# Optimization experiments

Measured on AMD Instinct MI355X. Metric: run time of the kernel, lower is better.

The kernel has to match this reference:

```python
import jax, jax.numpy as jnp
import numpy as np

D_MODEL = 256; N_LAYERS = 4; INPUT_LEN = 15
D_INNER = 512; D_STATE = 16; D_CONV = 4; DT_RANK = 16
BATCH = 4; SEQ = 2048; EPS = 1e-5

def _ln(x, w, b):
    m = jnp.mean(x, -1, keepdims=True)
    v = jnp.var(x, -1, keepdims=True)
    return (x - m) * jax.lax.rsqrt(v + EPS) * w + b

def _silu(x):
    return x * jax.nn.sigmoid(x)

def _mixer(h, inW, cw, cb, xpW, dtW, dtb, A_log, Dp, opW):
    # h: [B,L,d_model]
    xz = h @ inW.T                      # [B,L,2*D_INNER]
    xh, z = jnp.split(xz, 2, axis=-1)
    # causal depthwise conv1d
    xc = jnp.transpose(xh, (0, 2, 1))   # [B,D,L]
    xc = jax.lax.conv_general_dilated(xc, cw, (1,), [(D_CONV - 1, 0)],
                                      feature_group_count=D_INNER,
                                      dimension_numbers=('NCH', 'OIH', 'NCH'))
    xc = xc + cb[None, :, None]
    xh = _silu(jnp.transpose(xc, (0, 2, 1)))  # [B,L,D]
    dbl = xh @ xpW.T                    # [B,L,DT_RANK+2N]
    dt = dbl[..., :DT_RANK]
    Bm = dbl[..., DT_RANK:DT_RANK + D_STATE]
    C = dbl[..., DT_RANK + D_STATE:]
    dt = jax.nn.softplus(dt @ dtW.T + dtb)    # [B,L,D]
    A = -jnp.exp(A_log)                       # [D,N]
    dA = jnp.exp(dt[..., None] * A)           # [B,L,D,N]
    dBu = dt[..., None] * Bm[:, :, None, :] * xh[..., None]  # [B,L,D,N]
    def step(hst, inp):
        dA_t, dBu_t, C_t = inp
        hst = dA_t * hst + dBu_t
        y = jnp.einsum('bdn,bn->bd', hst, C_t)
        return hst, y
    h0 = jnp.zeros((xh.shape[0], D_INNER, D_STATE), xh.dtype)
    _, ys = jax.lax.scan(step, h0, (jnp.transpose(dA, (1, 0, 2, 3)),
                                    jnp.transpose(dBu, (1, 0, 2, 3)),
                                    jnp.transpose(C, (1, 0, 2))))
    y = jnp.transpose(ys, (1, 0, 2)) + Dp * xh
    y = y * _silu(z)
    return y @ opW.T

def setup_inputs():
    key = jax.random.key(0)
    ks = jax.random.split(key, 8)
    s = 0.02
    return {
        'x_src': jax.random.normal(ks[0], (BATCH, SEQ, INPUT_LEN), jnp.float32),
        'single_eval_pos': 1024,
        'in_W': jax.random.normal(ks[1], (D_MODEL, INPUT_LEN)) * s,
        'norm_w': jnp.ones((N_LAYERS, D_MODEL)),
        'norm_b': jnp.zeros((N_LAYERS, D_MODEL)),
        'inproj_W': jax.random.normal(ks[2], (N_LAYERS, 2 * D_INNER, D_MODEL)) * s,
        'conv_w': jax.random.normal(ks[3], (N_LAYERS, D_INNER, 1, D_CONV)) * 0.2,
        'conv_b': jnp.zeros((N_LAYERS, D_INNER)),
        'xproj_W': jax.random.normal(ks[4], (N_LAYERS, DT_RANK + 2 * D_STATE, D_INNER)) * s,
        'dtproj_W': jax.random.normal(ks[5], (N_LAYERS, D_INNER, DT_RANK)) * 0.1,
        'dtproj_b': jnp.log(jnp.expm1(jnp.full((N_LAYERS, D_INNER), 0.01))),
        'A_log': jnp.log(jnp.broadcast_to(jnp.arange(1, D_STATE + 1, dtype=jnp.float32), (N_LAYERS, D_INNER, D_STATE)) + 0.0),
        'D_param': jnp.ones((N_LAYERS, D_INNER)),
        'outproj_W': jax.random.normal(ks[6], (N_LAYERS, D_MODEL, D_INNER)) * s,
        'out_W': jax.random.normal(ks[7], (1, D_MODEL)) * s,
    }

def reference(x_src, single_eval_pos, in_W, norm_w, norm_b, inproj_W, conv_w, conv_b, xproj_W, dtproj_W, dtproj_b, A_log, D_param, outproj_W, out_W):
    h = x_src @ in_W.T                  # [B,L,d_model]
    res = None
    for i in range(N_LAYERS):
        res = h if res is None else h + res
        hn = _ln(res, norm_w[i], norm_b[i])
        h = _mixer(hn, inproj_W[i], conv_w[i], conv_b[i], xproj_W[i],
                   dtproj_W[i], dtproj_b[i], A_log[i], D_param[i], outproj_W[i])
    # backbone returns hidden_states directly (norm_f defined but not applied)
    return h @ out_W.T                  # [B,L,1]
```

## Files before the change

kernel.cpp:

```cpp
#include <hip/hip_runtime.h>

#define B_   4
#define T_   2048
#define BT_  8192
#define INL  15
#define DM   256
#define DI   512
#define DX   1024
#define DS_  16
#define DR_  16
#define NO_  48
#define NL   4
#define NC_  128
#define LCH  16

typedef short bf16x8 __attribute__((ext_vector_type(8)));
typedef float f32x4  __attribute__((ext_vector_type(4)));

__device__ __forceinline__ float sigmoidf_(float x){
    return __builtin_amdgcn_rcpf(1.f + __expf(-x));
}
__device__ __forceinline__ float softplusf_(float x){
    return fmaxf(x, 0.f) + __logf(1.f + __expf(-fabsf(x)));
}

__device__ __forceinline__ unsigned short f2bf(float x){
    union { float f; unsigned u; } v; v.f = x;
    unsigned r = (v.u + 0x7FFFu + ((v.u >> 16) & 1u)) >> 16;
    return (unsigned short)r;
}
__device__ __forceinline__ float bf2f(unsigned short h){
    union { unsigned u; float f; } v; v.u = ((unsigned)h) << 16;
    return v.f;
}

__device__ __forceinline__ void ld16(const float* __restrict__ p, float* v){
    const float4* q = (const float4*)p;
    float4 x0=q[0],x1=q[1],x2=q[2],x3=q[3];
    v[0]=x0.x; v[1]=x0.y; v[2]=x0.z; v[3]=x0.w;
    v[4]=x1.x; v[5]=x1.y; v[6]=x1.z; v[7]=x1.w;
    v[8]=x2.x; v[9]=x2.y; v[10]=x2.z; v[11]=x2.w;
    v[12]=x3.x; v[13]=x3.y; v[14]=x3.z; v[15]=x3.w;
}
__device__ __forceinline__ void st16(float* __restrict__ p, const float* v){
    float4* q = (float4*)p;
    q[0] = make_float4(v[0],v[1],v[2],v[3]);
    q[1] = make_float4(v[4],v[5],v[6],v[7]);
    q[2] = make_float4(v[8],v[9],v[10],v[11]);
    q[3] = make_float4(v[12],v[13],v[14],v[15]);
}

__global__ void k_cvtW3(const float* __restrict__ W0, unsigned short* __restrict__ h0,
                        unsigned short* __restrict__ l0, int n0,
                        const float* __restrict__ W1, unsigned short* __restrict__ h1,
                        unsigned short* __restrict__ l1, int n1,
                        const float* __restrict__ W2, unsigned short* __restrict__ h2,
                        unsigned short* __restrict__ l2, int n2){
    int g = blockIdx.x*256 + threadIdx.x;
    const float* W; unsigned short *hi, *lo; int idx;
    if(g < n0){ W = W0; hi = h0; lo = l0; idx = g; }
    else if(g < n0+n1){ W = W1; hi = h1; lo = l1; idx = g - n0; }
    else if(g < n0+n1+n2){ W = W2; hi = h2; lo = l2; idx = g - n0 - n1; }
    else return;
    float4 v = ((const float4*)W)[idx];
    ushort4 h, l;
    h.x = f2bf(v.x); l.x = f2bf(v.x - bf2f(h.x));
    h.y = f2bf(v.y); l.y = f2bf(v.y - bf2f(h.y));
    h.z = f2bf(v.z); l.z = f2bf(v.z - bf2f(h.z));
    h.w = f2bf(v.w); l.w = f2bf(v.w - bf2f(h.w));
    ((ushort4*)hi)[idx] = h;
    ((ushort4*)lo)[idx] = l;
}

__global__ void k_wcomb(const float* __restrict__ opW, const float* __restrict__ outW,
                        float* __restrict__ cw){
    int k = blockIdx.x*256 + threadIdx.x;
    float s = 0.f;
#pragma unroll 8
    for(int m=0;m<DM;m++) s += outW[m]*opW[(size_t)m*DI + k];
    cw[k] = s;
}

__global__ void k_inln(const float* __restrict__ x, const float* __restrict__ W,
                       float* __restrict__ res,
                       unsigned short* __restrict__ hnhi, unsigned short* __restrict__ hnlo,
                       const float* __restrict__ w, const float* __restrict__ b){
    int wv = threadIdx.x >> 6, lane = threadIdx.x & 63;
    int bt = blockIdx.x*4 + wv;
    const float* xr = x + bt*INL;
    float xl[INL];
#pragma unroll
    for(int k=0;k<INL;k++) xl[k] = xr[k];
    float4 v;
    float* vv = (float*)&v;
#pragma unroll
    for(int j=0;j<4;j++){
        int m = lane*4 + j;
        const float* wr = W + m*INL;
        float acc = 0.f;
#pragma unroll
        for(int k=0;k<INL;k++) acc += xl[k]*wr[k];
        vv[j] = acc;
    }
    ((float4*)(res + (size_t)bt*DM))[lane] = v;
    float s  = v.x+v.y+v.z+v.w;
    float ss = v.x*v.x+v.y*v.y+v.z*v.z+v.w*v.w;
#pragma unroll
    for(int m=1;m<64;m<<=1){ s += __shfl_xor(s,m); ss += __shfl_xor(ss,m); }
    float mean = s*(1.f/DM);
    float var  = ss*(1.f/DM) - mean*mean;
    float inv  = rsqrtf(var + 1e-5f);
    float4 wt = ((const float4*)w)[lane];
    float4 bs = ((const float4*)b)[lane];
    float4 o;
    o.x = (v.x-mean)*inv*wt.x + bs.x;
    o.y = (v.y-mean)*inv*wt.y + bs.y;
    o.z = (v.z-mean)*inv*wt.z + bs.z;
    o.w = (v.w-mean)*inv*wt.w + bs.w;
    ushort4 hh, ll;
    hh.x = f2bf(o.x); ll.x = f2bf(o.x - bf2f(hh.x));
    hh.y = f2bf(o.y); ll.y = f2bf(o.y - bf2f(hh.y));
    hh.z = f2bf(o.z); ll.z = f2bf(o.z - bf2f(hh.z));
    hh.w = f2bf(o.w); ll.w = f2bf(o.w - bf2f(hh.w));
    ((ushort4*)(hnhi + (size_t)bt*DM))[lane] = hh;
    ((ushort4*)(hnlo + (size_t)bt*DM))[lane] = ll;
}

__global__ void k_resln(const float* __restrict__ h, float* __restrict__ res,
                        unsigned short* __restrict__ hnhi, unsigned short* __restrict__ hnlo,
                        const float* __restrict__ w, const float* __restrict__ b, int storeRes){
    int wv = threadIdx.x >> 6, lane = threadIdx.x & 63;
    int bt = blockIdx.x*4 + wv;
    float4 v = ((const float4*)(h + (size_t)bt*DM))[lane];
    {
        float4 r = ((const float4*)(res + (size_t)bt*DM))[lane];
        v.x+=r.x; v.y+=r.y; v.z+=r.z; v.w+=r.w;
    }
    if(storeRes)
        ((float4*)(res + (size_t)bt*DM))[lane] = v;
    float s  = v.x+v.y+v.z+v.w;
    float ss = v.x*v.x+v.y*v.y+v.z*v.z+v.w*v.w;
#pragma unroll
    for(int m=1;m<64;m<<=1){ s += __shfl_xor(s,m); ss += __shfl_xor(ss,m); }
    float mean = s*(1.f/DM);
    float var  = ss*(1.f/DM) - mean*mean;
    float inv  = rsqrtf(var + 1e-5f);
    float4 wt = ((const float4*)w)[lane];
    float4 bs = ((const float4*)b)[lane];
    float4 o;
    o.x = (v.x-mean)*inv*wt.x + bs.x;
    o.y = (v.y-mean)*inv*wt.y + bs.y;
    o.z = (v.z-mean)*inv*wt.z + bs.z;
    o.w = (v.w-mean)*inv*wt.w + bs.w;
    ushort4 hh, ll;
    hh.x = f2bf(o.x); ll.x = f2bf(o.x - bf2f(hh.x));
    hh.y = f2bf(o.y); ll.y = f2bf(o.y - bf2f(hh.y));
    hh.z = f2bf(o.z); ll.z = f2bf(o.z - bf2f(hh.z));
    hh.w = f2bf(o.w); ll.w = f2bf(o.w - bf2f(hh.w));
    ((ushort4*)(hnhi + (size_t)bt*DM))[lane] = hh;
    ((ushort4*)(hnlo + (size_t)bt*DM))[lane] = ll;
}

template<int BM,int BN>
__global__ void __launch_bounds__(256) k_gemm_bf3(
    const unsigned short* __restrict__ Ahi, const unsigned short* __restrict__ Alo,
    const unsigned short* __restrict__ Bhi, const unsigned short* __restrict__ Blo,
    float* __restrict__ C, int M, int N, int K)
{
    constexpr int LDP = 40;
    constexpr int WM = BM/2, WN = BN/2;
    constexpr int MI_ = WM/16, NI_ = WN/16;
    __shared__ unsigned short sAh[BM*LDP], sAl[BM*LDP], sBh[BN*LDP], sBl[BN*LDP];
    int tid  = threadIdx.x;
    int wave = tid >> 6, lane = tid & 63;
    int wm0  = (wave >> 1) * WM, wn0 = (wave & 1) * WN;
    int m0   = blockIdx.y * BM, n0 = blockIdx.x * BN;
    int lr   = lane & 15;
    int kq   = (lane >> 4) * 8;
    int quad4 = (lane >> 4) * 4;

    f32x4 acc[MI_][NI_];
#pragma unroll
    for(int i=0;i<MI_;i++)
#pragma unroll
        for(int j=0;j<NI_;j++) acc[i][j] = (f32x4){0.f,0.f,0.f,0.f};

    for(int k0=0;k0<K;k0+=32){
#pragma unroll
        for(int i=tid;i<BM*4;i+=256){
            int r = i>>2, cg = (i&3)*8;
            size_t go = (size_t)(m0+r)*K + k0 + cg;
            *(float4*)(&sAh[r*LDP + cg]) = *(const float4*)(Ahi + go);
            *(float4*)(&sAl[r*LDP + cg]) = *(const float4*)(Alo + go);
        }
#pragma unroll
        for(int i=tid;i<BN*4;i+=256){
            int r = i>>2, cg = (i&3)*8;
            size_t go = (size_t)(n0+r)*K + k0 + cg;
            *(float4*)(&sBh[r*LDP + cg]) = *(const float4*)(Bhi + go);
            *(float4*)(&sBl[r*LDP + cg]) = *(const float4*)(Blo + go);
        }
        __syncthreads();
        bf16x8 ah[MI_], al[MI_], bh[NI_], bl[NI_];
#pragma unroll
        for(int mi=0;mi<MI_;mi++){
            int ro = (wm0 + mi*16 + lr)*LDP + kq;
            ah[mi] = *(const bf16x8*)(&sAh[ro]);
            al[mi] = *(const bf16x8*)(&sAl[ro]);
        }
#pragma unroll
        for(int ni=0;ni<NI_;ni++){
            int ro = (wn0 + ni*16 + lr)*LDP + kq;
            bh[ni] = *(const bf16x8*)(&sBh[ro]);
            bl[ni] = *(const bf16x8*)(&sBl[ro]);
        }
#pragma unroll
        for(int mi=0;mi<MI_;mi++)
#pragma unroll
            for(int ni=0;ni<NI_;ni++){
                acc[mi][ni] = __builtin_amdgcn_mfma_f32_16x16x32_bf16(ah[mi], bh[ni], acc[mi][ni], 0,0,0);
                acc[mi][ni] = __builtin_amdgcn_mfma_f32_16x16x32_bf16(ah[mi], bl[ni], acc[mi][ni], 0,0,0);
                acc[mi][ni] = __builtin_amdgcn_mfma_f32_16x16x32_bf16(al[mi], bh[ni], acc[mi][ni], 0,0,0);
            }
        __syncthreads();
    }
#pragma unroll
    for(int mi=0;mi<MI_;mi++)
#pragma unroll
        for(int ni=0;ni<NI_;ni++){
            int col = n0 + wn0 + ni*16 + lr;
#pragma unroll
            for(int r=0;r<4;r++){
                int row = m0 + wm0 + mi*16 + quad4 + r;
                C[(size_t)row*N + col] = acc[mi][ni][r];
            }
        }
}

template<int BM,int BN>
__global__ void __launch_bounds__(256) k_gemm_pk(
    const unsigned* __restrict__ Apk,
    const unsigned short* __restrict__ Bhi, const unsigned short* __restrict__ Blo,
    float* __restrict__ C, int M, int N, int K)
{
    constexpr int LDP = 40;
    constexpr int WM = BM/2, WN = BN/2;
    constexpr int MI_ = WM/16, NI_ = WN/16;
    __shared__ unsigned short sAh[BM*LDP], sAl[BM*LDP], sBh[BN*LDP], sBl[BN*LDP];
    int tid  = threadIdx.x;
    int wave = tid >> 6, lane = tid & 63;
    int wm0  = (wave >> 1) * WM, wn0 = (wave & 1) * WN;
    int m0   = blockIdx.y * BM, n0 = blockIdx.x * BN;
    int lr   = lane & 15;
    int kq   = (lane >> 4) * 8;
    int quad4 = (lane >> 4) * 4;

    f32x4 acc[MI_][NI_];
#pragma unroll
    for(int i=0;i<MI_;i++)
#pragma unroll
        for(int j=0;j<NI_;j++) acc[i][j] = (f32x4){0.f,0.f,0.f,0.f};

    for(int k0=0;k0<K;k0+=32){
#pragma unroll
        for(int i=tid;i<BM*2;i+=256){
            int r = i>>1, hf = (i&1)*16;
            const uint4* yp = (const uint4*)(Apk + (size_t)(m0+r)*K + k0 + hf);
#pragma unroll
            for(int q=0;q<4;q++){
                uint4 p = yp[q];
                ushort4 H, L;
                H.x=(unsigned short)p.x;  L.x=(unsigned short)(p.x>>16);
                H.y=(unsigned short)p.y;  L.y=(unsigned short)(p.y>>16);
                H.z=(unsigned short)p.z;  L.z=(unsigned short)(p.z>>16);
                H.w=(unsigned short)p.w;  L.w=(unsigned short)(p.w>>16);
                *(ushort4*)(&sAh[r*LDP + hf + q*4]) = H;
                *(ushort4*)(&sAl[r*LDP + hf + q*4]) = L;
            }
        }
#pragma unroll
        for(int i=tid;i<BN*4;i+=256){
            int r = i>>2, cg = (i&3)*8;
            size_t go = (size_t)(n0+r)*K + k0 + cg;
            *(float4*)(&sBh[r*LDP + cg]) = *(const float4*)(Bhi + go);
            *(float4*)(&sBl[r*LDP + cg]) = *(const float4*)(Blo + go);
        }
        __syncthreads();
        bf16x8 ah[MI_], al[MI_], bh[NI_], bl[NI_];
#pragma unroll
        for(int mi=0;mi<MI_;mi++){
            int ro = (wm0 + mi*16 + lr)*LDP + kq;
            ah[mi] = *(const bf16x8*)(&sAh[ro]);
            al[mi] = *(const bf16x8*)(&sAl[ro]);
        }
#pragma unroll
        for(int ni=0;ni<NI_;ni++){
            int ro = (wn0 + ni*16 + lr)*LDP + kq;
            bh[ni] = *(const bf16x8*)(&sBh[ro]);
            bl[ni] = *(const bf16x8*)(&sBl[ro]);
        }
#pragma unroll
        for(int mi=0;mi<MI_;mi++)
#pragma unroll
            for(int ni=0;ni<NI_;ni++){
                acc[mi][ni] = __builtin_amdgcn_mfma_f32_16x16x32_bf16(ah[mi], bh[ni], acc[mi][ni], 0,0,0);
                acc[mi][ni] = __builtin_amdgcn_mfma_f32_16x16x32_bf16(ah[mi], bl[ni], acc[mi][ni], 0,0,0);
                acc[mi][ni] = __builtin_amdgcn_mfma_f32_16x16x32_bf16(al[mi], bh[ni], acc[mi][ni], 0,0,0);
            }
        __syncthreads();
    }
#pragma unroll
    for(int mi=0;mi<MI_;mi++)
#pragma unroll
        for(int ni=0;ni<NI_;ni++){
            int col = n0 + wn0 + ni*16 + lr;
#pragma unroll
            for(int r=0;r<4;r++){
                int row = m0 + wm0 + mi*16 + quad4 + r;
                C[(size_t)row*N + col] = acc[mi][ni][r];
            }
        }
}

__global__ void __launch_bounds__(512) k_convxp2(
    const float* __restrict__ xz, const float* __restrict__ cw, const float* __restrict__ cb,
    const unsigned short* __restrict__ Bhi, const unsigned short* __restrict__ Blo,
    const float* __restrict__ dtW, const float* __restrict__ dtbias,
    const float* __restrict__ A_log,
    float* __restrict__ dbl,
    float* __restrict__ S, float* __restrict__ sdt)
{
    __shared__ unsigned short sAh[16*520], sAl[16*520];
    __shared__ float sP[6][16][20];
    __shared__ float sD[16*52];

    int tid = threadIdx.x;
    int wave = tid >> 6, lane = tid & 63;
    int lr = lane & 15, kq = (lane>>4)*8, quad4 = (lane>>4)*4;
    int m0 = blockIdx.x * LCH;
    int d  = tid;
    int nt = wave >> 1, kh = wave & 1;

    float xv[19];
    {
        int rbase = m0 - 3;
        bool mask0 = ((m0 & (T_-1)) == 0);
#pragma unroll
        for(int j=0;j<19;j++)
            xv[j] = (mask0 && j<3) ? 0.f : xz[(size_t)(rbase+j)*DX + d];
    }
    float a_[16]; ld16(A_log + (size_t)d*16, a_);
    float wr_[16]; ld16(dtW + (size_t)d*16, wr_);
    float bsv = dtbias[d];
    float4 w4 = *(const float4*)(cw + d*4);
    float bias = cb[d];
    float vh[16];
#pragma unroll
    for(int t=0;t<16;t++){
        float a = bias + w4.x*xv[t] + w4.y*xv[t+1] + w4.z*xv[t+2] + w4.w*xv[t+3];
        float v = a * sigmoidf_(a);
        vh[t] = v;
        unsigned short hh = f2bf(v);
        sAh[t*520 + d] = hh;
        sAl[t*520 + d] = f2bf(v - bf2f(hh));
    }
    __syncthreads();

    if(wave < 6){
        const unsigned short* bhp = Bhi + (size_t)(nt*16 + lr)*DI + kh*256 + kq;
        const unsigned short* blp = Blo + (size_t)(nt*16 + lr)*DI + kh*256 + kq;
        f32x4 acc = {0.f,0.f,0.f,0.f};
#pragma unroll 4
        for(int ks=0;ks<8;ks++){
            int ao = lr*520 + kh*256 + ks*32 + kq;
            bf16x8 ah = *(const bf16x8*)(&sAh[ao]);
            bf16x8 al = *(const bf16x8*)(&sAl[ao]);
            bf16x8 bh = *(const bf16x8*)(bhp + ks*32);
            bf16x8 bl = *(const bf16x8*)(blp + ks*32);
            acc = __builtin_amdgcn_mfma_f32_16x16x32_bf16(ah, bh, acc, 0,0,0);
            acc = __builtin_amdgcn_mfma_f32_16x16x32_bf16(ah, bl, acc, 0,0,0);
            acc = __builtin_amdgcn_mfma_f32_16x16x32_bf16(al, bh, acc, 0,0,0);
        }
#pragma unroll
        for(int r=0;r<4;r++) sP[wave][quad4+r][lr] = acc[r];
    }
    __syncthreads();

    for(int i=tid;i<768;i+=512){
        int t = i/48, n = i - t*48;
        int nt2 = n >> 4, nn = n & 15;
        float v = sP[nt2*2][t][nn] + sP[nt2*2+1][t][nn];
        dbl[(size_t)(m0+t)*48 + n] = v;
        sD[t*52 + n] = v;
    }
    __syncthreads();

#pragma unroll
    for(int n=0;n<16;n++) a_[n] = -__expf(a_[n]);
    int b = m0 >> 11;
    int c = (m0 & (T_-1)) >> 4;
    float st_[16];
#pragma unroll
    for(int n=0;n<16;n++) st_[n] = 0.f;
    float sd = 0.f;
#pragma unroll 4
    for(int t=0;t<16;t++){
        float dl[16]; ld16(&sD[t*52], dl);
        float bv[16]; ld16(&sD[t*52 + 16], bv);
        float pre = bsv;
#pragma unroll
        for(int r=0;r<16;r++) pre += dl[r]*wr_[r];
        float dtv = softplusf_(pre);
        float dx = dtv*vh[t];
        sd += dtv;
#pragma unroll
        for(int n=0;n<16;n++) st_[n] = __expf(dtv*a_[n])*st_[n] + dx*bv[n];
    }
    st16(S + (((size_t)b*NC_ + c)*DI + d)*16, st_);
    sdt[((size_t)b*NC_ + c)*DI + d] = sd;
}

__global__ void k_scan2(const float* __restrict__ S, const float* __restrict__ sdt,
                        const float* __restrict__ A_log, float* __restrict__ Hinit){
    int g = blockIdx.x*256 + threadIdx.x;
    int b = g >> 13;
    int dn = g & 8191;
    int d = dn >> 4;
    float a = -__expf(A_log[dn]);
    float H = 0.f;
    for(int c0=0;c0<NC_;c0+=8){
        float sv[8], gv[8];
#pragma unroll
        for(int j=0;j<8;j++){
            sv[j] = S[((size_t)(b*NC_ + c0 + j))*8192 + dn];
            gv[j] = sdt[(size_t)(b*NC_ + c0 + j)*DI + d];
        }
#pragma unroll
        for(int j=0;j<8;j++){
            size_t o = ((size_t)(b*NC_ + c0 + j))*8192 + dn;
            Hinit[o] = H;
            H = __expf(gv[j]*a)*H + sv[j];
        }
    }
}

__global__ void __launch_bounds__(256) k_scan3(
    const float* __restrict__ dbl, const float* __restrict__ xz,
    const float* __restrict__ cvw, const float* __restrict__ cvb,
    const float* __restrict__ A_log, const float* __restrict__ Dpar,
    const float* __restrict__ dtW, const float* __restrict__ dtbias,
    const float* __restrict__ Hinit, unsigned* __restrict__ Y)
{
    __shared__ float sbc[16*52];
    int tid = threadIdx.x;
    int c = blockIdx.y, b = blockIdx.z;
    int m0 = b*T_ + c*LCH;
    if(tid < 192){
        int t = tid/12, s = tid - t*12;
        *(float4*)(&sbc[t*52 + s*4]) = *(const float4*)(dbl + (size_t)(m0+t)*48 + s*4);
    }
    __syncthreads();
    int d = blockIdx.x*256 + tid;
    float xv[19];
    {
        int rbase = m0 - 3;
        bool mask0 = (c == 0);
#pragma unroll
        for(int j=0;j<19;j++)
            xv[j] = (mask0 && j<3) ? 0.f : xz[(size_t)(rbase+j)*DX + d];
    }
    float zvp[16];
#pragma unroll
    for(int t=0;t<16;t++) zvp[t] = xz[(size_t)(m0+t)*DX + DI + d];
    float4 w4 = *(const float4*)(cvw + d*4);
    float bias = cvb[d];
    float xhp[16];
#pragma unroll
    for(int t=0;t<16;t++){
        float a = bias + w4.x*xv[t] + w4.y*xv[t+1] + w4.z*xv[t+2] + w4.w*xv[t+3];
        xhp[t] = a * sigmoidf_(a);
    }
    float a_[16]; ld16(A_log + (size_t)d*16, a_);
#pragma unroll
    for(int n=0;n<16;n++) a_[n] = -__expf(a_[n]);
    float wr_[16]; ld16(dtW + (size_t)d*16, wr_);
    float bsv = dtbias[d];
    float st_[16]; ld16(Hinit + (((size_t)b*NC_ + c)*DI + d)*16, st_);
    float Dp = Dpar[d];
#pragma unroll 2
    for(int t=0;t<LCH;t++){
        int bt = m0 + t;
        float dl[16]; ld16(&sbc[t*52], dl);
        float bv[16]; ld16(&sbc[t*52 + 16], bv);
        float cv[16]; ld16(&sbc[t*52 + 32], cv);
        float pre = bsv;
#pragma unroll
        for(int r=0;r<16;r++) pre += dl[r]*wr_[r];
        float dtv = softplusf_(pre);
        float xhv = xhp[t];
        float dx = dtv*xhv;
        float y = 0.f;
#pragma unroll
        for(int n=0;n<16;n++){
            st_[n] = __expf(dtv*a_[n])*st_[n] + dx*bv[n];
            y += st_[n]*cv[n];
        }
        float zv = zvp[t];
        y += Dp*xhv;
        y = y * zv * sigmoidf_(zv);
        unsigned short hh = f2bf(y);
        unsigned short ll = f2bf(y - bf2f(hh));
        Y[(size_t)bt*DI + d] = (unsigned)hh | ((unsigned)ll << 16);
    }
}

__global__ void __launch_bounds__(512) k_scan3o(
    const float* __restrict__ dbl, const float* __restrict__ xz,
    const float* __restrict__ cvw, const float* __restrict__ cvb,
    const float* __restrict__ A_log, const float* __restrict__ Dpar,
    const float* __restrict__ dtW, const float* __restrict__ dtbias,
    const float* __restrict__ Hinit, const float* __restrict__ cwc,
    float* __restrict__ out)
{
    __shared__ float sbc[16*52];
    __shared__ float sW[8][16];
    int tid = threadIdx.x;
    int c = blockIdx.x, b = blockIdx.y;
    int m0 = b*T_ + c*LCH;
    if(tid < 192){
        int t = tid/12, s = tid - t*12;
        *(float4*)(&sbc[t*52 + s*4]) = *(const float4*)(dbl + (size_t)(m0+t)*48 + s*4);
    }
    __syncthreads();
    int d = tid;
    int wave = tid >> 6, lane = tid & 63;
    float xv[19];
    {
        int rbase = m0 - 3;
        bool mask0 = (c == 0);
#pragma unroll
        for(int j=0;j<19;j++)
            xv[j] = (mask0 && j<3) ? 0.f : xz[(size_t)(rbase+j)*DX + d];
    }
    float zvp[16];
#pragma unroll
    for(int t=0;t<16;t++) zvp[t] = xz[(size_t)(m0+t)*DX + DI + d];
    float4 w4 = *(const float4*)(cvw + d*4);
    float bias = cvb[d];
    float xhp[16];
#pragma unroll
    for(int t=0;t<16;t++){
        float a = bias + w4.x*xv[t] + w4.y*xv[t+1] + w4.z*xv[t+2] + w4.w*xv[t+3];
        xhp[t] = a * sigmoidf_(a);
    }
    float a_[16]; ld16(A_log + (size_t)d*16, a_);
#pragma unroll
    for(int n=0;n<16;n++) a_[n] = -__expf(a_[n]);
    float wr_[16]; ld16(dtW + (size_t)d*16, wr_);
    float bsv = dtbias[d];
    float st_[16]; ld16(Hinit + (((size_t)b*NC_ + c)*DI + d)*16, st_);
    float Dp = Dpar[d];
    float cwv = cwc[d];
#pragma unroll 2
    for(int t=0;t<LCH;t++){
        float dl[16]; ld16(&sbc[t*52], dl);
        float bv[16]; ld16(&sbc[t*52 + 16], bv);
        float cv[16]; ld16(&sbc[t*52 + 32], cv);
        float pre = bsv;
#pragma unroll
        for(int r=0;r<16;r++) pre += dl[r]*wr_[r];
        float dtv = softplusf_(pre);
        float xhv = xhp[t];
        float dx = dtv*xhv;
        float y = 0.f;
#pragma unroll
        for(int n=0;n<16;n++){
            st_[n] = __expf(dtv*a_[n])*st_[n] + dx*bv[n];
            y += st_[n]*cv[n];
        }
        float zv = zvp[t];
        y += Dp*xhv;
        y = y * zv * sigmoidf_(zv);
        float s = y * cwv;
#pragma unroll
        for(int m=1;m<64;m<<=1) s += __shfl_xor(s,m);
        if(lane==0) sW[wave][t] = s;
    }
    __syncthreads();
    if(tid < 16){
        float s = 0.f;
#pragma unroll
        for(int w=0;w<8;w++) s += sW[w][tid];
        out[m0 + tid] = s;
    }
}

extern "C" void kernel_launch(void* const* d_in, const int* in_sizes, int n_in,
                              void* d_out, int out_size, void* d_ws, size_t ws_size,
                              hipStream_t stream){
    const float* x_src    = (const float*)d_in[0];
    const float* in_W     = (const float*)d_in[2];
    const float* norm_w   = (const float*)d_in[3];
    const float* norm_b   = (const float*)d_in[4];
    const float* inproj_W = (const float*)d_in[5];
    const float* conv_w   = (const float*)d_in[6];
    const float* conv_b   = (const float*)d_in[7];
    const float* xproj_W  = (const float*)d_in[8];
    const float* dtproj_W = (const float*)d_in[9];
    const float* dtproj_b = (const float*)d_in[10];
    const float* A_log    = (const float*)d_in[11];
    const float* D_param  = (const float*)d_in[12];
    const float* outproj_W= (const float*)d_in[13];
    const float* out_W    = (const float*)d_in[14];

    float* ws  = (float*)d_ws;
    float* h    = ws;
    float* res  = h    + (size_t)BT_*DM;
    float* xz   = res  + (size_t)BT_*DM;
    float* dbl  = xz   + (size_t)BT_*DX;
    float* sdtb = dbl  + (size_t)BT_*48;
    float* Sbuf = sdtb + (size_t)B_*NC_*DI;
    float* Hbuf = Sbuf + (size_t)B_*NC_*DI*DS_;
    unsigned short* us = (unsigned short*)(Hbuf + (size_t)B_*NC_*DI*DS_);
    unsigned short* WhiIn  = us;
    unsigned short* WloIn  = WhiIn  + (size_t)NL*DX*DM;
    unsigned short* WhiOut = WloIn  + (size_t)NL*DX*DM;
    unsigned short* WloOut = WhiOut + (size_t)NL*DM*DI;
    unsigned short* WhiXp  = WloOut + (size_t)NL*DM*DI;
    unsigned short* WloXp  = WhiXp  + (size_t)NL*NO_*DI;
    unsigned short* hnhi   = WloXp  + (size_t)NL*NO_*DI;
    unsigned short* hnlo   = hnhi   + (size_t)BT_*DM;
    unsigned*       ybuf   = (unsigned*)(hnlo + (size_t)BT_*DM);
    float*          cwb    = (float*)(ybuf + (size_t)BT_*DI);

    int n0 = NL*DX*DM/4, n1 = NL*DM*DI/4, n2 = NL*NO_*DI/4;
    k_cvtW3<<<(n0+n1+n2 + 255)/256, 256, 0, stream>>>(
        inproj_W,  WhiIn,  WloIn,  n0,
        outproj_W, WhiOut, WloOut, n1,
        xproj_W,   WhiXp,  WloXp,  n2);
    k_wcomb<<<2, 256, 0, stream>>>(outproj_W + (size_t)3*DM*DI, out_W, cwb);
    k_inln<<<BT_/4, 256, 0, stream>>>(x_src, in_W, res, hnhi, hnlo, norm_w, norm_b);
    for(int i=0;i<NL;i++){
        if(i > 0)
            k_resln<<<BT_/4, 256, 0, stream>>>(h, res, hnhi, hnlo,
                norm_w + i*DM, norm_b + i*DM, (i < NL-1) ? 1 : 0);
        k_gemm_bf3<128,128><<<dim3(DX/128, BT_/128), 256, 0, stream>>>(
            hnhi, hnlo, WhiIn + (size_t)i*DX*DM, WloIn + (size_t)i*DX*DM, xz, BT_, DX, DM);
        k_convxp2<<<BT_/LCH, 512, 0, stream>>>(xz, conv_w + i*DI*4, conv_b + i*DI,
            WhiXp + (size_t)i*NO_*DI, WloXp + (size_t)i*NO_*DI,
            dtproj_W + (size_t)i*DI*DR_, dtproj_b + i*DI,
            A_log + (size_t)i*DI*DS_, dbl, Sbuf, sdtb);
        k_scan2<<<B_*DI*DS_/256, 256, 0, stream>>>(Sbuf, sdtb, A_log + (size_t)i*DI*DS_, Hbuf);
        if(i < NL-1){
            k_scan3<<<dim3(2, NC_, B_), 256, 0, stream>>>(dbl, xz,
                conv_w + i*DI*4, conv_b + i*DI,
                A_log + (size_t)i*DI*DS_, D_param + i*DI,
                dtproj_W + (size_t)i*DI*DR_, dtproj_b + i*DI, Hbuf, ybuf);
            k_gemm_pk<128,64><<<dim3(DM/64, BT_/128), 256, 0, stream>>>(
                ybuf, WhiOut + (size_t)i*DM*DI, WloOut + (size_t)i*DM*DI, h, BT_, DM, DI);
        } else {
            k_scan3o<<<dim3(NC_, B_), 512, 0, stream>>>(dbl, xz,
                conv_w + i*DI*4, conv_b + i*DI,
                A_log + (size_t)i*DI*DS_, D_param + i*DI,
                dtproj_W + (size_t)i*DI*DR_, dtproj_b + i*DI, Hbuf, cwb,
                (float*)d_out);
        }
    }
}
```

Baseline: 553.6 us.

## Fuse out-projection GEMM with residual add and LayerNorm; merge weight-combine into convert kernel

The out-projection GEMM now computes full 256-wide rows per block (32 rows by 256 columns), stages the results in XOR-swizzled shared memory, and applies the residual add plus the next layer's LayerNorm in its epilogue, writing the bf16 hi/lo split directly. This removes the separate k_resln launch and the round trip of the h buffer through global memory each layer. The small k_wcomb kernel is folded into the tail blocks of the weight-conversion kernel to save a launch. The trade-off is a narrower M tile, so every block reloads the full 256x512 B matrix, and a grid of 256 blocks may underfill the GPU.

```diff
diff --git a/kernel.cpp b/kernel.cpp
--- a/kernel.cpp
+++ b/kernel.cpp
@@ -55,13 +55,24 @@
                         const float* __restrict__ W1, unsigned short* __restrict__ h1,
                         unsigned short* __restrict__ l1, int n1,
                         const float* __restrict__ W2, unsigned short* __restrict__ h2,
-                        unsigned short* __restrict__ l2, int n2){
+                        unsigned short* __restrict__ l2, int n2,
+                        const float* __restrict__ opW3, const float* __restrict__ outW,
+                        float* __restrict__ cwc){
     int g = blockIdx.x*256 + threadIdx.x;
     const float* W; unsigned short *hi, *lo; int idx;
     if(g < n0){ W = W0; hi = h0; lo = l0; idx = g; }
     else if(g < n0+n1){ W = W1; hi = h1; lo = l1; idx = g - n0; }
     else if(g < n0+n1+n2){ W = W2; hi = h2; lo = l2; idx = g - n0 - n1; }
-    else return;
+    else {
+        int k = g - (n0+n1+n2);
+        if(k < DI){
+            float s = 0.f;
+#pragma unroll 8
+            for(int m=0;m<DM;m++) s += outW[m]*opW3[(size_t)m*DI + k];
+            cwc[k] = s;
+        }
+        return;
+    }
     float4 v = ((const float4*)W)[idx];
     ushort4 h, l;
     h.x = f2bf(v.x); l.x = f2bf(v.x - bf2f(h.x));
@@ -70,15 +81,6 @@
     h.w = f2bf(v.w); l.w = f2bf(v.w - bf2f(h.w));
     ((ushort4*)hi)[idx] = h;
     ((ushort4*)lo)[idx] = l;
-}
-
-__global__ void k_wcomb(const float* __restrict__ opW, const float* __restrict__ outW,
-                        float* __restrict__ cw){
-    int k = blockIdx.x*256 + threadIdx.x;
-    float s = 0.f;
-#pragma unroll 8
-    for(int m=0;m<DM;m++) s += outW[m]*opW[(size_t)m*DI + k];
-    cw[k] = s;
 }
 
 __global__ void k_inln(const float* __restrict__ x, const float* __restrict__ W,
@@ -126,41 +128,6 @@
     ((ushort4*)(hnlo + (size_t)bt*DM))[lane] = ll;
 }
 
-__global__ void k_resln(const float* __restrict__ h, float* __restrict__ res,
-                        unsigned short* __restrict__ hnhi, unsigned short* __restrict__ hnlo,
-                        const float* __restrict__ w, const float* __restrict__ b, int storeRes){
-    int wv = threadIdx.x >> 6, lane = threadIdx.x & 63;
-    int bt = blockIdx.x*4 + wv;
-    float4 v = ((const float4*)(h + (size_t)bt*DM))[lane];
-    {
-        float4 r = ((const float4*)(res + (size_t)bt*DM))[lane];
-        v.x+=r.x; v.y+=r.y; v.z+=r.z; v.w+=r.w;
-    }
-    if(storeRes)
-        ((float4*)(res + (size_t)bt*DM))[lane] = v;
-    float s  = v.x+v.y+v.z+v.w;
-    float ss = v.x*v.x+v.y*v.y+v.z*v.z+v.w*v.w;
-#pragma unroll
-    for(int m=1;m<64;m<<=1){ s += __shfl_xor(s,m); ss += __shfl_xor(ss,m); }
-    float mean = s*(1.f/DM);
-    float var  = ss*(1.f/DM) - mean*mean;
-    float inv  = rsqrtf(var + 1e-5f);
-    float4 wt = ((const float4*)w)[lane];
-    float4 bs = ((const float4*)b)[lane];
-    float4 o;
-    o.x = (v.x-mean)*inv*wt.x + bs.x;
-    o.y = (v.y-mean)*inv*wt.y + bs.y;
-    o.z = (v.z-mean)*inv*wt.z + bs.z;
-    o.w = (v.w-mean)*inv*wt.w + bs.w;
-    ushort4 hh, ll;
-    hh.x = f2bf(o.x); ll.x = f2bf(o.x - bf2f(hh.x));
-    hh.y = f2bf(o.y); ll.y = f2bf(o.y - bf2f(hh.y));
-    hh.z = f2bf(o.z); ll.z = f2bf(o.z - bf2f(hh.z));
-    hh.w = f2bf(o.w); ll.w = f2bf(o.w - bf2f(hh.w));
-    ((ushort4*)(hnhi + (size_t)bt*DM))[lane] = hh;
-    ((ushort4*)(hnlo + (size_t)bt*DM))[lane] = ll;
-}
-
 template<int BM,int BN>
 __global__ void __launch_bounds__(256) k_gemm_bf3(
     const unsigned short* __restrict__ Ahi, const unsigned short* __restrict__ Alo,
@@ -188,17 +155,17 @@
     for(int k0=0;k0<K;k0+=32){
 #pragma unroll
         for(int i=tid;i<BM*4;i+=256){
-            int r = i>>2, cg = (i&3)*8;
-            size_t go = (size_t)(m0+r)*K + k0 + cg;
-            *(float4*)(&sAh[r*LDP + cg]) = *(const float4*)(Ahi + go);
-            *(float4*)(&sAl[r*LDP + cg]) = *(const float4*)(Alo + go);
+            int r = i>>2, cg2 = (i&3)*8;
+            size_t go = (size_t)(m0+r)*K + k0 + cg2;
+            *(float4*)(&sAh[r*LDP + cg2]) = *(const float4*)(Ahi + go);
+            *(float4*)(&sAl[r*LDP + cg2]) = *(const float4*)(Alo + go);
         }
 #pragma unroll
         for(int i=tid;i<BN*4;i+=256){
-            int r = i>>2, cg = (i&3)*8;
-            size_t go = (size_t)(n0+r)*K + k0 + cg;
-            *(float4*)(&sBh[r*LDP + cg]) = *(const float4*)(Bhi + go);
-            *(float4*)(&sBl[r*LDP + cg]) = *(const float4*)(Blo + go);
+            int r = i>>2, cg2 = (i&3)*8;
+            size_t go = (size_t)(n0+r)*K + k0 + cg2;
+            *(float4*)(&sBh[r*LDP + cg2]) = *(const float4*)(Bhi + go);
+            *(float4*)(&sBl[r*LDP + cg2]) = *(const float4*)(Blo + go);
         }
         __syncthreads();
         bf16x8 ah[MI_], al[MI_], bh[NI_], bl[NI_];
@@ -237,29 +204,33 @@
         }
 }
 
-template<int BM,int BN>
-__global__ void __launch_bounds__(256) k_gemm_pk(
+__global__ void __launch_bounds__(256) k_gemm_pk_ln(
     const unsigned* __restrict__ Apk,
     const unsigned short* __restrict__ Bhi, const unsigned short* __restrict__ Blo,
-    float* __restrict__ C, int M, int N, int K)
+    float* __restrict__ res,
+    unsigned short* __restrict__ hnhi, unsigned short* __restrict__ hnlo,
+    const float* __restrict__ w, const float* __restrict__ b, int storeRes)
 {
-    constexpr int LDP = 40;
-    constexpr int WM = BM/2, WN = BN/2;
-    constexpr int MI_ = WM/16, NI_ = WN/16;
-    __shared__ unsigned short sAh[BM*LDP], sAl[BM*LDP], sBh[BN*LDP], sBl[BN*LDP];
+    constexpr int BM = 32, BN = 256, K = 512, LDP = 40;
+    __shared__ __align__(16) char smem[(BM*LDP + BM*LDP + BN*LDP + BN*LDP)*2];
+    unsigned short* sAh = (unsigned short*)smem;
+    unsigned short* sAl = sAh + BM*LDP;
+    unsigned short* sBh = sAl + BM*LDP;
+    unsigned short* sBl = sBh + BN*LDP;
+    float* sH = (float*)smem;
+
     int tid  = threadIdx.x;
     int wave = tid >> 6, lane = tid & 63;
-    int wm0  = (wave >> 1) * WM, wn0 = (wave & 1) * WN;
-    int m0   = blockIdx.y * BM, n0 = blockIdx.x * BN;
+    int wm0  = (wave >> 1) * 16;
+    int wn0  = (wave & 1) * 128;
+    int m0   = blockIdx.x * BM;
     int lr   = lane & 15;
     int kq   = (lane >> 4) * 8;
     int quad4 = (lane >> 4) * 4;
 
-    f32x4 acc[MI_][NI_];
-#pragma unroll
-    for(int i=0;i<MI_;i++)
-#pragma unroll
-        for(int j=0;j<NI_;j++) acc[i][j] = (f32x4){0.f,0.f,0.f,0.f};
+    f32x4 acc[8];
+#pragma unroll
+    for(int j=0;j<8;j++) acc[j] = (f32x4){0.f,0.f,0.f,0.f};
 
     for(int k0=0;k0<K;k0+=32){
 #pragma unroll
@@ -280,46 +251,79 @@
         }
 #pragma unroll
         for(int i=tid;i<BN*4;i+=256){
-            int r = i>>2, cg = (i&3)*8;
-            size_t go = (size_t)(n0+r)*K + k0 + cg;
-            *(float4*)(&sBh[r*LDP + cg]) = *(const float4*)(Bhi + go);
-            *(float4*)(&sBl[r*LDP + cg]) = *(const float4*)(Blo + go);
+            int r = i>>2, cg2 = (i&3)*8;
+            size_t go = (size_t)r*K + k0 + cg2;
+            *(float4*)(&sBh[r*LDP + cg2]) = *(const float4*)(Bhi + go);
+            *(float4*)(&sBl[r*LDP + cg2]) = *(const float4*)(Blo + go);
         }
         __syncthreads();
-        bf16x8 ah[MI_], al[MI_], bh[NI_], bl[NI_];
-#pragma unroll
-        for(int mi=0;mi<MI_;mi++){
-            int ro = (wm0 + mi*16 + lr)*LDP + kq;
-            ah[mi] = *(const bf16x8*)(&sAh[ro]);
-            al[mi] = *(const bf16x8*)(&sAl[ro]);
-        }
-#pragma unroll
-        for(int ni=0;ni<NI_;ni++){
-            int ro = (wn0 + ni*16 + lr)*LDP + kq;
-            bh[ni] = *(const bf16x8*)(&sBh[ro]);
-            bl[ni] = *(const bf16x8*)(&sBl[ro]);
-        }
-#pragma unroll
-        for(int mi=0;mi<MI_;mi++)
-#pragma unroll
-            for(int ni=0;ni<NI_;ni++){
-                acc[mi][ni] = __builtin_amdgcn_mfma_f32_16x16x32_bf16(ah[mi], bh[ni], acc[mi][ni], 0,0,0);
-                acc[mi][ni] = __builtin_amdgcn_mfma_f32_16x16x32_bf16(ah[mi], bl[ni], acc[mi][ni], 0,0,0);
-                acc[mi][ni] = __builtin_amdgcn_mfma_f32_16x16x32_bf16(al[mi], bh[ni], acc[mi][ni], 0,0,0);
-            }
+        int ro = (wm0 + lr)*LDP + kq;
+        bf16x8 ah = *(const bf16x8*)(&sAh[ro]);
+        bf16x8 al = *(const bf16x8*)(&sAl[ro]);
+#pragma unroll
+        for(int ni=0;ni<8;ni++){
+            int rb = (wn0 + ni*16 + lr)*LDP + kq;
+            bf16x8 bh = *(const bf16x8*)(&sBh[rb]);
+            bf16x8 bl = *(const bf16x8*)(&sBl[rb]);
+            acc[ni] = __builtin_amdgcn_mfma_f32_16x16x32_bf16(ah, bh, acc[ni], 0,0,0);
+            acc[ni] = __builtin_amdgcn_mfma_f32_16x16x32_bf16(ah, bl, acc[ni], 0,0,0);
+            acc[ni] = __builtin_amdgcn_mfma_f32_16x16x32_bf16(al, bh, acc[ni], 0,0,0);
+        }
         __syncthreads();
     }
-#pragma unroll
-    for(int mi=0;mi<MI_;mi++)
-#pragma unroll
-        for(int ni=0;ni<NI_;ni++){
-            int col = n0 + wn0 + ni*16 + lr;
-#pragma unroll
-            for(int r=0;r<4;r++){
-                int row = m0 + wm0 + mi*16 + quad4 + r;
-                C[(size_t)row*N + col] = acc[mi][ni][r];
-            }
-        }
+
+#pragma unroll
+    for(int ni=0;ni<8;ni++){
+#pragma unroll
+        for(int r=0;r<4;r++){
+            int rowl = wm0 + quad4 + r;
+            int col  = wn0 + ni*16 + lr;
+            sH[rowl*256 + (col ^ ((rowl&7)<<2))] = acc[ni][r];
+        }
+    }
+    __syncthreads();
+
+    int row = tid >> 3, sub = tid & 7;
+    int gr  = m0 + row;
+    float v[32];
+    float s = 0.f, ss = 0.f;
+    const float4* rp = (const float4*)(res + (size_t)gr*DM + sub*32);
+#pragma unroll
+    for(int k=0;k<8;k++){
+        int kk = k ^ (row & 7);
+        float4 hv = *(float4*)&sH[row*256 + sub*32 + kk*4];
+        float4 rv = rp[k];
+        float4 t;
+        t.x = hv.x + rv.x; t.y = hv.y + rv.y; t.z = hv.z + rv.z; t.w = hv.w + rv.w;
+        v[k*4+0]=t.x; v[k*4+1]=t.y; v[k*4+2]=t.z; v[k*4+3]=t.w;
+        s  += t.x+t.y+t.z+t.w;
+        ss += t.x*t.x + t.y*t.y + t.z*t.z + t.w*t.w;
+    }
+#pragma unroll
+    for(int m=1;m<8;m<<=1){ s += __shfl_xor(s,m); ss += __shfl_xor(ss,m); }
+    float mean = s*(1.f/DM);
+    float var  = ss*(1.f/DM) - mean*mean;
+    float inv  = rsqrtf(var + 1e-5f);
+#pragma unroll
+    for(int k=0;k<8;k++){
+        float4 wt = ((const float4*)(w + sub*32))[k];
+        float4 bs = ((const float4*)(b + sub*32))[k];
+        float4 o;
+        o.x = (v[k*4+0]-mean)*inv*wt.x + bs.x;
+        o.y = (v[k*4+1]-mean)*inv*wt.y + bs.y;
+        o.z = (v[k*4+2]-mean)*inv*wt.z + bs.z;
+        o.w = (v[k*4+3]-mean)*inv*wt.w + bs.w;
+        ushort4 hh, ll;
+        hh.x = f2bf(o.x); ll.x = f2bf(o.x - bf2f(hh.x));
+        hh.y = f2bf(o.y); ll.y = f2bf(o.y - bf2f(hh.y));
+        hh.z = f2bf(o.z); ll.z = f2bf(o.z - bf2f(hh.z));
+        hh.w = f2bf(o.w); ll.w = f2bf(o.w - bf2f(hh.w));
+        *(ushort4*)(hnhi + (size_t)gr*DM + sub*32 + k*4) = hh;
+        *(ushort4*)(hnlo + (size_t)gr*DM + sub*32 + k*4) = ll;
+        if(storeRes)
+            *(float4*)(res + (size_t)gr*DM + sub*32 + k*4) =
+                make_float4(v[k*4+0], v[k*4+1], v[k*4+2], v[k*4+3]);
+    }
 }
 
 __global__ void __launch_bounds__(512) k_convxp2(
@@ -614,8 +618,7 @@
     const float* out_W    = (const float*)d_in[14];
 
     float* ws  = (float*)d_ws;
-    float* h    = ws;
-    float* res  = h    + (size_t)BT_*DM;
+    float* res  = ws;
     float* xz   = res  + (size_t)BT_*DM;
     float* dbl  = xz   + (size_t)BT_*DX;
     float* sdtb = dbl  + (size_t)BT_*48;
@@ -634,16 +637,14 @@
     float*          cwb    = (float*)(ybuf + (size_t)BT_*DI);
 
     int n0 = NL*DX*DM/4, n1 = NL*DM*DI/4, n2 = NL*NO_*DI/4;
-    k_cvtW3<<<(n0+n1+n2 + 255)/256, 256, 0, stream>>>(
+    int nTot = n0 + n1 + n2;
+    k_cvtW3<<<(nTot + DI + 255)/256, 256, 0, stream>>>(
         inproj_W,  WhiIn,  WloIn,  n0,
         outproj_W, WhiOut, WloOut, n1,
-        xproj_W,   WhiXp,  WloXp,  n2);
-    k_wcomb<<<2, 256, 0, stream>>>(outproj_W + (size_t)3*DM*DI, out_W, cwb);
+        xproj_W,   WhiXp,  WloXp,  n2,
+        outproj_W + (size_t)3*DM*DI, out_W, cwb);
     k_inln<<<BT_/4, 256, 0, stream>>>(x_src, in_W, res, hnhi, hnlo, norm_w, norm_b);
     for(int i=0;i<NL;i++){
-        if(i > 0)
-            k_resln<<<BT_/4, 256, 0, stream>>>(h, res, hnhi, hnlo,
-                norm_w + i*DM, norm_b + i*DM, (i < NL-1) ? 1 : 0);
         k_gemm_bf3<128,128><<<dim3(DX/128, BT_/128), 256, 0, stream>>>(
             hnhi, hnlo, WhiIn + (size_t)i*DX*DM, WloIn + (size_t)i*DX*DM, xz, BT_, DX, DM);
         k_convxp2<<<BT_/LCH, 512, 0, stream>>>(xz, conv_w + i*DI*4, conv_b + i*DI,
@@ -656,8 +657,10 @@
                 conv_w + i*DI*4, conv_b + i*DI,
                 A_log + (size_t)i*DI*DS_, D_param + i*DI,
                 dtproj_W + (size_t)i*DI*DR_, dtproj_b + i*DI, Hbuf, ybuf);
-            k_gemm_pk<128,64><<<dim3(DM/64, BT_/128), 256, 0, stream>>>(
-                ybuf, WhiOut + (size_t)i*DM*DI, WloOut + (size_t)i*DM*DI, h, BT_, DM, DI);
+            k_gemm_pk_ln<<<BT_/32, 256, 0, stream>>>(
+                ybuf, WhiOut + (size_t)i*DM*DI, WloOut + (size_t)i*DM*DI,
+                res, hnhi, hnlo, norm_w + (i+1)*DM, norm_b + (i+1)*DM,
+                (i < NL-2) ? 1 : 0);
         } else {
             k_scan3o<<<dim3(NC_, B_), 512, 0, stream>>>(dbl, xz,
                 conv_w + i*DI*4, conv_b + i*DI,
```

New measurement: 592.6 us. +7.0%, slower.
